# Optimization experiments

Measured on AMD Instinct MI355X. Metric: run time of the kernel, lower is better.

The kernel has to match this reference:

```python
import jax, jax.numpy as jnp
import numpy as np

V, E, H, L = 50257, 512, 512, 2
PAD_ID = 50256


def setup_inputs() -> dict:
    key = jax.random.key(0)
    ks = jax.random.split(key, 24)
    B, TD, TE = 16, 64, 256
    s = 0.02
    emb = jax.random.normal(ks[0], (V, E), jnp.float32) * s
    emb = emb.at[PAD_ID].set(0.0)  # padding_idx row is zero
    inp = {
        "dec_input_ids": jax.random.randint(ks[1], (B, TD), 0, V, jnp.int32),
        "initial_hidden": jax.random.normal(ks[2], (L, B, H), jnp.float32),
        "initial_cell": jax.random.normal(ks[3], (L, B, H), jnp.float32),
        "encoder_outputs": jax.random.normal(ks[4], (B, TE, H), jnp.float32),
        "src_mask": jax.random.randint(ks[5], (B, TE), 0, 2, jnp.int32),
        "emb": emb,
        "W1_w": jax.random.normal(ks[6], (H, H), jnp.float32) * s,
        "W1_b": jnp.zeros((H,), jnp.float32),
        "W2_w": jax.random.normal(ks[7], (H, H), jnp.float32) * s,
        "W2_b": jnp.zeros((H,), jnp.float32),
        "v_w": jax.random.normal(ks[8], (H,), jnp.float32) * s,
        "v_b": jnp.zeros((), jnp.float32),
        "W_ih0": jax.random.normal(ks[9], (4 * H, E + H), jnp.float32) * s,
        "W_hh0": jax.random.normal(ks[10], (4 * H, H), jnp.float32) * s,
        "b_ih0": jnp.zeros((4 * H,), jnp.float32),
        "b_hh0": jnp.zeros((4 * H,), jnp.float32),
        "W_ih1": jax.random.normal(ks[11], (4 * H, H), jnp.float32) * s,
        "W_hh1": jax.random.normal(ks[12], (4 * H, H), jnp.float32) * s,
        "b_ih1": jnp.zeros((4 * H,), jnp.float32),
        "b_hh1": jnp.zeros((4 * H,), jnp.float32),
        "fc_w": jax.random.normal(ks[13], (V, H), jnp.float32) * s,
        "fc_b": jnp.zeros((V,), jnp.float32),
    }
    return inp


def _lstm_cell(x, h, c, Wi, Wh, bi, bh):
    g = x @ Wi.T + bi + h @ Wh.T + bh  # (B, 4H)
    i, f, gg, o = jnp.split(g, 4, axis=-1)  # PyTorch gate order i,f,g,o
    i, f, o = jax.nn.sigmoid(i), jax.nn.sigmoid(f), jax.nn.sigmoid(o)
    gg = jnp.tanh(gg)
    cn = f * c + i * gg
    hn = o * jnp.tanh(cn)
    return hn, cn


def reference(dec_input_ids, initial_hidden, initial_cell, encoder_outputs, src_mask,
              emb, W1_w, W1_b, W2_w, W2_b, v_w, v_b,
              W_ih0, W_hh0, b_ih0, b_hh0, W_ih1, W_hh1, b_ih1, b_hh1,
              fc_w, fc_b):
    embedded = emb[dec_input_ids]                      # (B, T_dec, E)
    enc_proj = encoder_outputs @ W1_w.T + W1_b         # W1(encoder_outputs), (B, T_enc, H)
    pad = src_mask == 0                                # (B, T_enc)
    layers = ((W_ih0, W_hh0, b_ih0, b_hh0), (W_ih1, W_hh1, b_ih1, b_hh1))

    def step(carry, emb_t):
        h, c = carry                                   # each (L, B, H)
        q = h[-1] @ W2_w.T + W2_b                      # (B, H)
        score = jnp.tanh(enc_proj + q[:, None, :]) @ v_w + v_b  # (B, T_enc)
        score = jnp.where(pad, -1e9, score)
        attn = jax.nn.softmax(score, axis=-1)
        context = jnp.einsum('bt,bth->bh', attn, encoder_outputs)
        x = jnp.concatenate([emb_t, context], axis=-1)  # (B, E+H)
        hs, cs = [], []
        for l, (Wi, Wh, bi, bh) in enumerate(layers):
            hn, cn = _lstm_cell(x, h[l], c[l], Wi, Wh, bi, bh)
            hs.append(hn); cs.append(cn)
            x = hn
        logits_t = x @ fc_w.T + fc_b                    # (B, V)
        return (jnp.stack(hs), jnp.stack(cs)), logits_t

    _, logits = jax.lax.scan(step, (initial_hidden, initial_cell),
                             jnp.swapaxes(embedded, 0, 1))  # (T_dec, B, V)
    return jnp.swapaxes(logits, 0, 1)                       # (B, T_dec, V)
```

## Files before the change

kernel.cpp:

```cpp
#include <hip/hip_runtime.h>

#define DI __device__ __forceinline__

typedef __attribute__((ext_vector_type(2))) float f32x2;
typedef __attribute__((ext_vector_type(4))) float f32x4;
typedef __attribute__((ext_vector_type(8))) short bf16x8;
typedef __attribute__((ext_vector_type(8))) unsigned short u16x8;

constexpr int Vv = 50257, NPAD = 50304, Ee = 512, Hh = 512, Bb = 16, TDn = 64, TEn = 256;
constexpr int NBLK = 64;

constexpr size_t OFF_ENCP = 0;
constexpr size_t OFF_ENCT = OFF_ENCP + (size_t)Bb*TEn*Hh*4;
constexpr size_t OFF_G0E  = OFF_ENCT + (size_t)Bb*Hh*TEn*4;
constexpr size_t OFF_FCWB = OFF_G0E  + (size_t)TDn*Bb*4*Hh*4;
constexpr size_t OFF_H1B  = OFF_FCWB + (size_t)NPAD*Hh*2;
constexpr size_t OFF_Q    = OFF_H1B  + (size_t)TDn*Bb*Hh*2;
constexpr size_t OFF_SC   = OFF_Q    + (size_t)Bb*Hh*4;
constexpr size_t OFF_CTX  = OFF_SC   + (size_t)Bb*TEn*4;
constexpr size_t OFF_H0   = OFF_CTX  + (size_t)Bb*Hh*4;
constexpr size_t OFF_H1   = OFF_H0   + (size_t)2*Bb*Hh*4;
constexpr size_t OFF_SYNC = OFF_H1   + (size_t)2*Bb*Hh*4;

DI float dot4(f32x4 a, f32x4 b) { return a[0]*b[0] + a[1]*b[1] + a[2]*b[2] + a[3]*b[3]; }
DI float wsum(float v) { for (int m = 32; m; m >>= 1) v += __shfl_xor(v, m, 64); return v; }
DI float wmax(float v) { for (int m = 32; m; m >>= 1) v = fmaxf(v, __shfl_xor(v, m, 64)); return v; }
DI void wsum4(float& a, float& b, float& c, float& d) {
    #pragma unroll
    for (int m = 32; m; m >>= 1) {
        a += __shfl_xor(a, m, 64);
        b += __shfl_xor(b, m, 64);
        c += __shfl_xor(c, m, 64);
        d += __shfl_xor(d, m, 64);
    }
}
DI float tanhfast(float x) { float e = __expf(2.f * x); return 1.f - 2.f / (e + 1.f); }
DI float sigm(float x) { return 1.f / (1.f + __expf(-x)); }

DI int swz(int a) { return a ^ (((a >> 5) & 7) << 2); }

DI float gload1(const float* p) {
    return __hip_atomic_load(p, __ATOMIC_RELAXED, __HIP_MEMORY_SCOPE_AGENT);
}
DI void gstore1(float* p, float v) {
    __hip_atomic_store(p, v, __ATOMIC_RELAXED, __HIP_MEMORY_SCOPE_AGENT);
}
DI f32x2 gload2(const float* p) {
    unsigned long long u = __hip_atomic_load((const unsigned long long*)p,
                                             __ATOMIC_RELAXED, __HIP_MEMORY_SCOPE_AGENT);
    return __builtin_bit_cast(f32x2, u);
}
DI void gstore2(float* p, f32x2 v) {
    __hip_atomic_store((unsigned long long*)p, __builtin_bit_cast(unsigned long long, v),
                       __ATOMIC_RELAXED, __HIP_MEMORY_SCOPE_AGENT);
}
DI f32x4 gload4(const float* p) {
    f32x2 a = gload2(p), b = gload2(p + 2);
    f32x4 r; r[0] = a[0]; r[1] = a[1]; r[2] = b[0]; r[3] = b[1];
    return r;
}
DI void gstoreu16(unsigned short* p, unsigned short v) {
    __hip_atomic_store(p, v, __ATOMIC_RELAXED, __HIP_MEMORY_SCOPE_AGENT);
}

DI unsigned short f2bf(float f) {
    unsigned u = __builtin_bit_cast(unsigned, f);
    unsigned r = (u + 0x7FFFu + ((u >> 16) & 1u)) >> 16;
    return (unsigned short)r;
}
DI u16x8 cvt8(f32x4 a, f32x4 b) {
    u16x8 r;
    r[0]=f2bf(a[0]); r[1]=f2bf(a[1]); r[2]=f2bf(a[2]); r[3]=f2bf(a[3]);
    r[4]=f2bf(b[0]); r[5]=f2bf(b[1]); r[6]=f2bf(b[2]); r[7]=f2bf(b[3]);
    return r;
}

DI void gbar(char* sy, int bid, unsigned kg) {
    __syncthreads();
    if (threadIdx.x < 64) {
        unsigned long long* gf = (unsigned long long*)(sy + ((kg & 1) ? 0 : 512));
        if (threadIdx.x == 0) {
            asm volatile("s_waitcnt vmcnt(0)" ::: "memory");
            char* p = (char*)(gf + (size_t)(bid >> 3) * 8) + (bid & 7);
            __hip_atomic_store(p, (char)(unsigned char)kg, __ATOMIC_RELAXED, __HIP_MEMORY_SCOPE_AGENT);
        }
        const unsigned long long pat = 0x0101010101010101ULL * (unsigned char)kg;
        const int lane = threadIdx.x;
        for (;;) {
            bool ok = true;
            if (lane < 8)
                ok = (__hip_atomic_load(gf + (size_t)lane * 8, __ATOMIC_RELAXED,
                                        __HIP_MEMORY_SCOPE_AGENT) == pat);
            if (__all(ok)) break;
            __builtin_amdgcn_s_sleep(1);
        }
    }
    __syncthreads();
}

DI void rbar(char* sy, int g, int u4, unsigned kr) {
    __syncthreads();
    if (threadIdx.x == 0) {
        unsigned* gr = (unsigned*)(sy + ((kr & 1) ? 1024 : 2048));
        asm volatile("s_waitcnt vmcnt(0)" ::: "memory");
        char* p = (char*)(gr + (size_t)g * 16) + u4;
        __hip_atomic_store(p, (char)(unsigned char)kr, __ATOMIC_RELAXED, __HIP_MEMORY_SCOPE_AGENT);
        const unsigned pat = 0x01010101u * (unsigned char)kr;
        while (__hip_atomic_load(gr + (size_t)g * 16, __ATOMIC_RELAXED,
                                 __HIP_MEMORY_SCOPE_AGENT) != pat)
            __builtin_amdgcn_s_sleep(1);
    }
    __syncthreads();
}

__global__ void prep_fcw_kernel(const float* __restrict__ src, unsigned short* __restrict__ dst) {
    size_t i = ((size_t)blockIdx.x * 256 + threadIdx.x) << 3;
    int n = (int)(i >> 9);
    u16x8 v = {0,0,0,0,0,0,0,0};
    if (n < Vv) {
        const float* p = src + i;
        v = cvt8(*(const f32x4*)p, *(const f32x4*)(p + 4));
    }
    *(u16x8*)(dst + i) = v;
}

__global__ void transpose_kernel(const float* __restrict__ enc, float* __restrict__ encT) {
    __shared__ float tile[32][33];
    const int b = blockIdx.z, e0 = blockIdx.x << 5, h0 = blockIdx.y << 5;
    const int tx = threadIdx.x, ty = threadIdx.y;
    #pragma unroll
    for (int i = 0; i < 4; ++i)
        tile[ty + i*8][tx] = enc[((size_t)(b*TEn + e0 + ty + i*8))*Hh + h0 + tx];
    __syncthreads();
    #pragma unroll
    for (int i = 0; i < 4; ++i)
        encT[((size_t)(b*Hh + h0 + ty + i*8))*TEn + e0 + tx] = tile[tx][ty + i*8];
}

template<int SRCBF, int GATHER, int OUTM>
__global__ __launch_bounds__(256, 2) void gemm_bt(
    const void* __restrict__ Av, const void* __restrict__ Bv,
    const float* __restrict__ bias, const float* __restrict__ bias2,
    float* __restrict__ Cout, int M, int N, int K, int ldb,
    const int* __restrict__ ids, int NV)
{
    __shared__ unsigned short As[128*32], Bs[128*32];
    const int tid = threadIdx.x;
    const int bn = blockIdx.x, bm = blockIdx.y;
    const int w = tid >> 6, l = tid & 63;
    const int wm = w >> 1, wn = w & 1;
    const int lr = l & 15, ls = l >> 4;
    f32x4 acc[4][4] = {};

    const int r0 = tid >> 2, c0 = (tid & 3) << 3;

    for (int kb = 0; kb < K; kb += 32) {
        #pragma unroll
        for (int half = 0; half < 2; ++half) {
            const int rr = r0 + half*64;
            {
                const int gm = bm*128 + rr;
                size_t arow = GATHER ? (size_t)ids[((gm & 15) << 6) + (gm >> 4)] : (size_t)gm;
                u16x8 v;
                if (SRCBF) {
                    v = *(const u16x8*)((const unsigned short*)Av + arow*(size_t)K + kb + c0);
                } else {
                    const float* ap = (const float*)Av + arow*(size_t)K + kb + c0;
                    v = cvt8(*(const f32x4*)ap, *(const f32x4*)(ap + 4));
                }
                *(u16x8*)&As[rr*32 + c0] = v;
            }
            {
                const size_t brow = (size_t)(bn*128 + rr);
                u16x8 v;
                if (SRCBF) {
                    v = *(const u16x8*)((const unsigned short*)Bv + brow*(size_t)ldb + kb + c0);
                } else {
                    const float* bp = (const float*)Bv + brow*(size_t)ldb + kb + c0;
                    v = cvt8(*(const f32x4*)bp, *(const f32x4*)(bp + 4));
                }
                *(u16x8*)&Bs[rr*32 + c0] = v;
            }
        }
        __syncthreads();
        bf16x8 af[4], bfv[4];
        #pragma unroll
        for (int mt = 0; mt < 4; ++mt) af[mt]  = *(const bf16x8*)&As[(wm*64 + mt*16 + lr)*32 + ls*8];
        #pragma unroll
        for (int nt = 0; nt < 4; ++nt) bfv[nt] = *(const bf16x8*)&Bs[(wn*64 + nt*16 + lr)*32 + ls*8];
        #pragma unroll
        for (int mt = 0; mt < 4; ++mt)
            #pragma unroll
            for (int nt = 0; nt < 4; ++nt)
                acc[mt][nt] = __builtin_amdgcn_mfma_f32_16x16x32_bf16(af[mt], bfv[nt], acc[mt][nt], 0, 0, 0);
        __syncthreads();
    }

    #pragma unroll
    for (int mt = 0; mt < 4; ++mt) {
        #pragma unroll
        for (int nt = 0; nt < 4; ++nt) {
            const int n = bn*128 + wn*64 + nt*16 + lr;
            const int mbase = bm*128 + wm*64 + mt*16 + ls*4;
            f32x4 a = acc[mt][nt];
            #pragma unroll
            for (int r = 0; r < 4; ++r) {
                const int m = mbase + r;
                if (OUTM == 0) {
                    float v = a[r] + bias[n] + (bias2 ? bias2[n] : 0.f);
                    Cout[(size_t)m*N + n] = v;
                } else {
                    if (n < NV) {
                        float v = a[r] + bias[n];
                        Cout[(size_t)(((m & 15) << 6) + (m >> 4))*NV + n] = v;
                    }
                }
            }
        }
    }
}

__global__ __launch_bounds__(512, 1) void recur_kernel(
    const float* __restrict__ ih, const float* __restrict__ ic,
    const float* __restrict__ W2w, const float* __restrict__ W2b,
    const float* __restrict__ vw, const float* __restrict__ vb,
    const int* __restrict__ smask,
    const float* __restrict__ Wi0, const float* __restrict__ Wh0,
    const float* __restrict__ Wi1, const float* __restrict__ Wh1,
    const float* __restrict__ bi1, const float* __restrict__ bh1,
    char* __restrict__ ws)
{
    float* encP = (float*)(ws + OFF_ENCP);
    float* encT = (float*)(ws + OFF_ENCT);
    float* g0e  = (float*)(ws + OFF_G0E);
    unsigned short* h1bf = (unsigned short*)(ws + OFF_H1B);
    float* qb  = (float*)(ws + OFF_Q);
    float* sc  = (float*)(ws + OFF_SC);
    float* ctx = (float*)(ws + OFF_CTX);
    float* h0b = (float*)(ws + OFF_H0);
    float* h1v = (float*)(ws + OFF_H1);
    char* sy   = (char*)(ws + OFF_SYNC);

    __shared__ float lds[2 * Bb * Hh];

    const int tid = threadIdx.x, bid = blockIdx.x;
    const int wid = tid >> 6, l = tid & 63;
    const int j  = (bid << 3) + wid;
    const int k0 = l << 3;

    f32x4 wi0a[4], wi0b[4], wh0a[4], wh0b[4];
    f32x4 wi1a[4], wi1b[4], wh1a[4], wh1b[4];
    float bb1[4];
    #pragma unroll
    for (int g = 0; g < 4; ++g) {
        const float* p0 = Wi0 + (size_t)(g*Hh + j)*(Ee + Hh) + Ee + k0;
        wi0a[g] = *(const f32x4*)p0; wi0b[g] = *(const f32x4*)(p0 + 4);
        const float* p1 = Wh0 + (size_t)(g*Hh + j)*Hh + k0;
        wh0a[g] = *(const f32x4*)p1; wh0b[g] = *(const f32x4*)(p1 + 4);
        const float* p2 = Wi1 + (size_t)(g*Hh + j)*Hh + k0;
        wi1a[g] = *(const f32x4*)p2; wi1b[g] = *(const f32x4*)(p2 + 4);
        const float* p3 = Wh1 + (size_t)(g*Hh + j)*Hh + k0;
        wh1a[g] = *(const f32x4*)p3; wh1b[g] = *(const f32x4*)(p3 + 4);
        bb1[g] = bi1[g*Hh + j] + bh1[g*Hh + j];
    }
    const float* wr = W2w + (size_t)j*Hh + k0;
    const f32x4 w2a = *(const f32x4*)wr, w2d = *(const f32x4*)(wr + 4);
    const float w2bias = W2b[j];
    const f32x4 va = *(const f32x4*)&vw[k0], vd = *(const f32x4*)&vw[k0 + 4];
    const float vbias = vb[0];

    float c0r = (l < 16) ? ic[l*Hh + j]           : 0.f;
    float c1r = (l < 16) ? ic[Bb*Hh + l*Hh + j]   : 0.f;

    const int gb  = bid >> 2, u4 = bid & 3;
    const int se0 = u4*64 + wid*8;
    const int ch0 = u4*128 + wid*16;
    const int msk = (l < 8) ? smask[gb*TEn + se0 + l] : 1;

    for (int i = (bid*512 + tid)*4; i < Bb*Hh; i += NBLK*512*4) {
        gstore2(&h0b[i],     *(const f32x2*)&ih[i]);
        gstore2(&h0b[i + 2], *(const f32x2*)&ih[i + 2]);
        gstore2(&h1v[i],     *(const f32x2*)&ih[Bb*Hh + i]);
        gstore2(&h1v[i + 2], *(const f32x2*)&ih[Bb*Hh + i + 2]);
    }
    unsigned kg = 1, kr = 0;
    gbar(sy, bid, kg);

    for (int t = 0; t < TDn; ++t) {
        const int p = t & 1;
        const float* h1r = h1v + p*(Bb*Hh);
        float*       h1w = h1v + (p^1)*(Bb*Hh);
        const float* h0r = h0b + p*(Bb*Hh);
        float*       h0w = h0b + (p^1)*(Bb*Hh);

        float ge0 = 0.f, ge1 = 0.f, ge2 = 0.f, ge3 = 0.f;
        if (l < 16) {
            const float* gp = g0e + ((size_t)(t*Bb + l))*(4*Hh) + j;
            ge0 = gp[0]; ge1 = gp[Hh]; ge2 = gp[2*Hh]; ge3 = gp[3*Hh];
        }

        {
            for (int i = tid*4; i < Bb*Hh; i += 2048)
                *(f32x4*)&lds[swz(i)] = gload4(&h1r[i]);
            __syncthreads();
            float qv = 0.f;
            #pragma unroll 4
            for (int b = 0; b < Bb; ++b) {
                f32x4 ha = *(const f32x4*)&lds[swz(b*Hh + k0)];
                f32x4 hd = *(const f32x4*)&lds[swz(b*Hh + k0 + 4)];
                float s = dot4(ha, w2a) + dot4(hd, w2d);
                s = wsum(s);
                qv = (l == b) ? s + w2bias : qv;
            }
            if (l < 16) gstore1(&qb[l*Hh + j], qv);
        }
        gbar(sy, bid, ++kg);

        {
            if (tid < 128) *(f32x4*)&lds[tid*4] = gload4(&qb[gb*Hh + tid*4]);
            __syncthreads();
            f32x4 qa = *(const f32x4*)&lds[k0];
            f32x4 qd = *(const f32x4*)&lds[k0 + 4];
            float myS = 0.f;
            #pragma unroll
            for (int i = 0; i < 8; ++i) {
                const int e = se0 + i;
                const float* ep = encP + ((size_t)(gb*TEn + e))*Hh + k0;
                f32x4 ea = *(const f32x4*)ep, ed = *(const f32x4*)(ep + 4);
                float s = 0.f;
                #pragma unroll
                for (int c = 0; c < 4; ++c)
                    s += tanhfast(ea[c] + qa[c]) * va[c] + tanhfast(ed[c] + qd[c]) * vd[c];
                s = wsum(s);
                myS = (l == i) ? s : myS;
            }
            if (l < 8)
                gstore1(&sc[gb*TEn + se0 + l], (msk == 0) ? -1e9f : (myS + vbias));
        }
        rbar(sy, gb, u4, ++kr);

        {
            f32x4 s4 = gload4(&sc[gb*TEn + (l << 2)]);
            float mx = wmax(fmaxf(fmaxf(s4[0], s4[1]), fmaxf(s4[2], s4[3])));
            f32x4 e4; float sm = 0.f;
            #pragma unroll
            for (int c = 0; c < 4; ++c) { e4[c] = __expf(s4[c] - mx); sm += e4[c]; }
            sm = wsum(sm);
            const float inv = 1.0f / sm;
            float myC = 0.f;
            #pragma unroll 4
            for (int i = 0; i < 16; ++i) {
                const int h = ch0 + i;
                f32x4 en = *(const f32x4*)&encT[((size_t)(gb*Hh + h))*TEn + (l << 2)];
                float s = wsum(dot4(e4, en));
                myC = (l == i) ? s : myC;
            }
            if (l < 16) gstore1(&ctx[gb*Hh + ch0 + l], myC * inv);
        }
        gbar(sy, bid, ++kg);

        {
            for (int i = tid*4; i < Bb*Hh; i += 2048) {
                *(f32x4*)&lds[swz(i)]          = gload4(&ctx[i]);
                *(f32x4*)&lds[swz(Bb*Hh + i)]  = gload4(&h0r[i]);
            }
            __syncthreads();
            float ls0 = 0.f, ls1 = 0.f, ls2 = 0.f, ls3 = 0.f;
            #pragma unroll 4
            for (int b = 0; b < Bb; ++b) {
                f32x4 xa = *(const f32x4*)&lds[swz(b*Hh + k0)];
                f32x4 xd = *(const f32x4*)&lds[swz(b*Hh + k0 + 4)];
                f32x4 ha = *(const f32x4*)&lds[swz(Bb*Hh + b*Hh + k0)];
                f32x4 hd = *(const f32x4*)&lds[swz(Bb*Hh + b*Hh + k0 + 4)];
                float s0 = dot4(wi0a[0],xa)+dot4(wi0b[0],xd)+dot4(wh0a[0],ha)+dot4(wh0b[0],hd);
                float s1 = dot4(wi0a[1],xa)+dot4(wi0b[1],xd)+dot4(wh0a[1],ha)+dot4(wh0b[1],hd);
                float s2 = dot4(wi0a[2],xa)+dot4(wi0b[2],xd)+dot4(wh0a[2],ha)+dot4(wh0b[2],hd);
                float s3 = dot4(wi0a[3],xa)+dot4(wi0b[3],xd)+dot4(wh0a[3],ha)+dot4(wh0b[3],hd);
                wsum4(s0, s1, s2, s3);
                if (l == b) { ls0 = s0; ls1 = s1; ls2 = s2; ls3 = s3; }
            }
            if (l < 16) {
                float ii = sigm(ls0 + ge0), ff = sigm(ls1 + ge1);
                float gg = tanhfast(ls2 + ge2), oo = sigm(ls3 + ge3);
                float cn = ff*c0r + ii*gg;
                c0r = cn;
                gstore1(&h0w[l*Hh + j], oo * tanhfast(cn));
            }
        }
        gbar(sy, bid, ++kg);

        {
            for (int i = tid*4; i < Bb*Hh; i += 2048) {
                *(f32x4*)&lds[swz(i)]          = gload4(&h0w[i]);
                *(f32x4*)&lds[swz(Bb*Hh + i)]  = gload4(&h1r[i]);
            }
            __syncthreads();
            float ls0 = 0.f, ls1 = 0.f, ls2 = 0.f, ls3 = 0.f;
            #pragma unroll 4
            for (int b = 0; b < Bb; ++b) {
                f32x4 xa = *(const f32x4*)&lds[swz(b*Hh + k0)];
                f32x4 xd = *(const f32x4*)&lds[swz(b*Hh + k0 + 4)];
                f32x4 ha = *(const f32x4*)&lds[swz(Bb*Hh + b*Hh + k0)];
                f32x4 hd = *(const f32x4*)&lds[swz(Bb*Hh + b*Hh + k0 + 4)];
                float s0 = dot4(wi1a[0],xa)+dot4(wi1b[0],xd)+dot4(wh1a[0],ha)+dot4(wh1b[0],hd);
                float s1 = dot4(wi1a[1],xa)+dot4(wi1b[1],xd)+dot4(wh1a[1],ha)+dot4(wh1b[1],hd);
                float s2 = dot4(wi1a[2],xa)+dot4(wi1b[2],xd)+dot4(wh1a[2],ha)+dot4(wh1b[2],hd);
                float s3 = dot4(wi1a[3],xa)+dot4(wi1b[3],xd)+dot4(wh1a[3],ha)+dot4(wh1b[3],hd);
                wsum4(s0, s1, s2, s3);
                if (l == b) { ls0 = s0; ls1 = s1; ls2 = s2; ls3 = s3; }
            }
            if (l < 16) {
                float ii = sigm(ls0 + bb1[0]), ff = sigm(ls1 + bb1[1]);
                float gg = tanhfast(ls2 + bb1[2]), oo = sigm(ls3 + bb1[3]);
                float cn = ff*c1r + ii*gg;
                c1r = cn;
                float hn = oo * tanhfast(cn);
                gstore1(&h1w[l*Hh + j], hn);
                gstoreu16(&h1bf[((size_t)(t*Bb + l))*Hh + j], f2bf(hn));
            }
        }
        gbar(sy, bid, ++kg);
    }
}

extern "C" void kernel_launch(void* const* d_in, const int* in_sizes, int n_in,
                              void* d_out, int out_size, void* d_ws, size_t ws_size,
                              hipStream_t stream)
{
    const int*   ids  = (const int*)d_in[0];
    const float* ih   = (const float*)d_in[1];
    const float* ic   = (const float*)d_in[2];
    const float* enc  = (const float*)d_in[3];
    const int*   smask= (const int*)d_in[4];
    const float* emb  = (const float*)d_in[5];
    const float* W1w  = (const float*)d_in[6];
    const float* W1b  = (const float*)d_in[7];
    const float* W2w  = (const float*)d_in[8];
    const float* W2b  = (const float*)d_in[9];
    const float* vw   = (const float*)d_in[10];
    const float* vb   = (const float*)d_in[11];
    const float* Wi0  = (const float*)d_in[12];
    const float* Wh0  = (const float*)d_in[13];
    const float* bi0  = (const float*)d_in[14];
    const float* bh0  = (const float*)d_in[15];
    const float* Wi1  = (const float*)d_in[16];
    const float* Wh1  = (const float*)d_in[17];
    const float* bi1  = (const float*)d_in[18];
    const float* bh1  = (const float*)d_in[19];
    const float* fcw  = (const float*)d_in[20];
    const float* fcb  = (const float*)d_in[21];
    float* out = (float*)d_out;
    char*  ws  = (char*)d_ws;

    hipMemsetAsync(ws + OFF_SYNC, 0, 4096, stream);

    prep_fcw_kernel<<<dim3((unsigned)((size_t)NPAD*Hh/8/256)), dim3(256), 0, stream>>>(
        fcw, (unsigned short*)(ws + OFF_FCWB));

    transpose_kernel<<<dim3(TEn/32, Hh/32, Bb), dim3(32, 8), 0, stream>>>(
        enc, (float*)(ws + OFF_ENCT));

    gemm_bt<0,0,0><<<dim3(Hh/128, (Bb*TEn)/128), dim3(256), 0, stream>>>(
        enc, W1w, W1b, nullptr, (float*)(ws + OFF_ENCP),
        Bb*TEn, Hh, Hh, Hh, nullptr, 0);

    gemm_bt<0,1,0><<<dim3((4*Hh)/128, (TDn*Bb)/128), dim3(256), 0, stream>>>(
        emb, Wi0, bi0, bh0, (float*)(ws + OFF_G0E),
        TDn*Bb, 4*Hh, Ee, Ee + Hh, ids, 0);

    {
        void* args[] = { (void*)&ih, (void*)&ic, (void*)&W2w, (void*)&W2b,
                         (void*)&vw, (void*)&vb, (void*)&smask,
                         (void*)&Wi0, (void*)&Wh0, (void*)&Wi1, (void*)&Wh1,
                         (void*)&bi1, (void*)&bh1, (void*)&ws };
        hipLaunchCooperativeKernel((void*)recur_kernel, dim3(NBLK), dim3(512), args, 0, stream);
    }

    gemm_bt<1,0,1><<<dim3(NPAD/128, (TDn*Bb)/128), dim3(256), 0, stream>>>(
        ws + OFF_H1B, ws + OFF_FCWB, fcb, nullptr, out,
        TDn*Bb, NPAD, Hh, Hh, nullptr, Vv);
}
```

Measured before the change: 3.363 ms.

## Use master-block grid barrier with generation flags and remap batch groups

```diff
diff --git a/kernel.cpp b/kernel.cpp
--- a/kernel.cpp
+++ b/kernel.cpp
@@ -77,38 +77,50 @@
 
 DI void gbar(char* sy, int bid, unsigned kg) {
     __syncthreads();
-    if (threadIdx.x < 64) {
-        unsigned long long* gf = (unsigned long long*)(sy + ((kg & 1) ? 0 : 512));
-        if (threadIdx.x == 0) {
-            asm volatile("s_waitcnt vmcnt(0)" ::: "memory");
-            char* p = (char*)(gf + (size_t)(bid >> 3) * 8) + (bid & 7);
-            __hip_atomic_store(p, (char)(unsigned char)kg, __ATOMIC_RELAXED, __HIP_MEMORY_SCOPE_AGENT);
-        }
-        const unsigned long long pat = 0x0101010101010101ULL * (unsigned char)kg;
-        const int lane = threadIdx.x;
-        for (;;) {
-            bool ok = true;
-            if (lane < 8)
-                ok = (__hip_atomic_load(gf + (size_t)lane * 8, __ATOMIC_RELAXED,
-                                        __HIP_MEMORY_SCOPE_AGENT) == pat);
-            if (__all(ok)) break;
-            __builtin_amdgcn_s_sleep(1);
-        }
+    const size_t pofs = (kg & 1) ? 0 : 1024;
+    unsigned long long* arr = (unsigned long long*)(sy + pofs);
+    unsigned* gen = (unsigned*)(sy + 2048 + pofs);
+    const int tid = threadIdx.x;
+    if (tid == 0) {
+        asm volatile("s_waitcnt vmcnt(0)" ::: "memory");
+        char* p = (char*)(arr + (size_t)(bid >> 3) * 16) + (bid & 7);
+        __hip_atomic_store(p, (char)(unsigned char)kg, __ATOMIC_RELAXED, __HIP_MEMORY_SCOPE_AGENT);
+    }
+    if (bid == 0) {
+        if (tid < 64) {
+            const unsigned long long pat = 0x0101010101010101ULL * (unsigned char)kg;
+            for (;;) {
+                bool ok = true;
+                if (tid < 8)
+                    ok = (__hip_atomic_load(arr + (size_t)tid * 16, __ATOMIC_RELAXED,
+                                            __HIP_MEMORY_SCOPE_AGENT) == pat);
+                if (__all(ok)) break;
+                __builtin_amdgcn_s_sleep(2);
+            }
+            asm volatile("" ::: "memory");
+            if (tid < 8)
+                __hip_atomic_store(gen + (size_t)tid * 32, kg, __ATOMIC_RELAXED,
+                                   __HIP_MEMORY_SCOPE_AGENT);
+        }
+    } else if (tid == 0) {
+        unsigned* gp = gen + (size_t)(bid & 7) * 32;
+        while (__hip_atomic_load(gp, __ATOMIC_RELAXED, __HIP_MEMORY_SCOPE_AGENT) != kg)
+            __builtin_amdgcn_s_sleep(2);
     }
     __syncthreads();
 }
 
-DI void rbar(char* sy, int g, int u4, unsigned kr) {
+DI void rbar(char* sy, int gb, int u4, unsigned kr) {
     __syncthreads();
     if (threadIdx.x == 0) {
-        unsigned* gr = (unsigned*)(sy + ((kr & 1) ? 1024 : 2048));
+        const size_t pofs = (kr & 1) ? 4096 : 6144;
+        unsigned* w = (unsigned*)(sy + pofs) + (size_t)gb * 32;
         asm volatile("s_waitcnt vmcnt(0)" ::: "memory");
-        char* p = (char*)(gr + (size_t)g * 16) + u4;
-        __hip_atomic_store(p, (char)(unsigned char)kr, __ATOMIC_RELAXED, __HIP_MEMORY_SCOPE_AGENT);
+        __hip_atomic_store((char*)w + u4, (char)(unsigned char)kr, __ATOMIC_RELAXED,
+                           __HIP_MEMORY_SCOPE_AGENT);
         const unsigned pat = 0x01010101u * (unsigned char)kr;
-        while (__hip_atomic_load(gr + (size_t)g * 16, __ATOMIC_RELAXED,
-                                 __HIP_MEMORY_SCOPE_AGENT) != pat)
-            __builtin_amdgcn_s_sleep(1);
+        while (__hip_atomic_load(w, __ATOMIC_RELAXED, __HIP_MEMORY_SCOPE_AGENT) != pat)
+            __builtin_amdgcn_s_sleep(2);
     }
     __syncthreads();
 }
@@ -272,7 +284,7 @@
     float c0r = (l < 16) ? ic[l*Hh + j]           : 0.f;
     float c1r = (l < 16) ? ic[Bb*Hh + l*Hh + j]   : 0.f;
 
-    const int gb  = bid >> 2, u4 = bid & 3;
+    const int gb  = bid & 15, u4 = bid >> 4;
     const int se0 = u4*64 + wid*8;
     const int ch0 = u4*128 + wid*16;
     const int msk = (l < 8) ? smask[gb*TEn + se0 + l] : 1;
@@ -452,7 +464,7 @@
     float* out = (float*)d_out;
     char*  ws  = (char*)d_ws;
 
-    hipMemsetAsync(ws + OFF_SYNC, 0, 4096, stream);
+    hipMemsetAsync(ws + OFF_SYNC, 0, 8192, stream);
 
     prep_fcw_kernel<<<dim3((unsigned)((size_t)NPAD*Hh/8/256)), dim3(256), 0, stream>>>(
         fcw, (unsigned short*)(ws + OFF_FCWB));
```

New measurement: 3.181 ms. 5.4% less time.
